# Optimization experiments

Hardware: AMD Instinct MI355X
Metric: run time of the kernel (lower is better)

Reference implementation:

```python
import jax, jax.numpy as jnp
import numpy as np

P = 20000          # plan nodes (queries)
H = 128            # hidden_dim_plan
DIMS = {"table": (100000, 96), "pred": (400000, 160), "agg": (60000, 64), "join": (80000, 64)}
BN_EPS = 1e-5


def setup_inputs() -> dict:
    key = jax.random.key(0)
    ks = iter(jax.random.split(key, 32))
    inp = {}
    for t, (n, d) in DIMS.items():
        inp[f"feat_{t}"] = jax.random.normal(next(ks), (n, d), dtype=jnp.float32)
        inp[f"idx_{t}"] = jax.random.randint(next(ks), (n,), 0, P)
        # per-type encoder: Linear(d, H) (stored as [d, H])
        inp[f"W_{t}"] = jax.random.normal(next(ks), (d, H), dtype=jnp.float32) * 0.02
        inp[f"b_{t}"] = jnp.zeros((H,), jnp.float32)
    # est head: BatchNorm1d(4H) -> Linear(4H,H)+ReLU -> Linear(H,H)+ReLU -> Linear(H,1)
    inp["bn_gamma"] = jnp.ones((4 * H,), jnp.float32)
    inp["bn_beta"] = jnp.zeros((4 * H,), jnp.float32)
    inp["W1"] = jax.random.normal(next(ks), (4 * H, H), dtype=jnp.float32) * 0.02
    inp["b1"] = jnp.zeros((H,), jnp.float32)
    inp["W2"] = jax.random.normal(next(ks), (H, H), dtype=jnp.float32) * 0.02
    inp["b2"] = jnp.zeros((H,), jnp.float32)
    inp["W3"] = jax.random.normal(next(ks), (H, 1), dtype=jnp.float32) * 0.02
    inp["b3"] = jnp.zeros((1,), jnp.float32)
    inp["num_plan"] = P
    return inp


def _seg_mean(x, idx, num_seg):
    # DGL mean pooling: mean over incoming edges, 0 for nodes with no edges
    s = jax.ops.segment_sum(x, idx, num_segments=num_seg)
    c = jax.ops.segment_sum(jnp.ones((x.shape[0], 1), x.dtype), idx, num_segments=num_seg)
    return s / jnp.maximum(c, 1.0)


def _forward(feats, idxs, params, num_plan):
    pooled = []
    for t in ("table", "pred", "agg", "join"):
        enc = jax.nn.relu(feats[t] @ params[f"W_{t}"] + params[f"b_{t}"])  # [N_t, H]
        pooled.append(_seg_mean(enc, idxs[t], num_plan))                    # [P, H]
    x = jnp.concatenate(pooled, axis=1)  # [P, 4H]
    # BatchNorm1d (training mode: batch statistics, biased variance)
    mu = jnp.mean(x, axis=0)
    var = jnp.mean(jnp.square(x - mu), axis=0)
    x = (x - mu) * jax.lax.rsqrt(var + BN_EPS) * params["bn_gamma"] + params["bn_beta"]
    x = jax.nn.relu(x @ params["W1"] + params["b1"])
    x = jax.nn.relu(x @ params["W2"] + params["b2"])
    return x @ params["W3"] + params["b3"]  # [P, 1]


def reference(feat_table, feat_pred, feat_agg, feat_join,
              W_table, b_table, W_pred, b_pred, W_agg, b_agg, W_join, b_join,
              bn_gamma, bn_beta, W1, b1, W2, b2, W3, b3,
              idx_table, idx_pred, idx_agg, idx_join, num_plan):
    feats = {"table": feat_table, "pred": feat_pred, "agg": feat_agg, "join": feat_join}
    idxs = {"table": idx_table, "pred": idx_pred, "agg": idx_agg, "join": idx_join}
    params = dict(W_table=W_table, b_table=b_table, W_pred=W_pred, b_pred=b_pred,
                  W_agg=W_agg, b_agg=b_agg, W_join=W_join, b_join=b_join,
                  bn_gamma=bn_gamma, bn_beta=bn_beta, W1=W1, b1=b1, W2=W2, b2=b2, W3=W3, b3=b3)
    return _forward(feats, idxs, params, num_plan)
```

## Files before the change

kernel.cpp:

```cpp
#include <hip/hip_runtime.h>
#include <cstdint>


constexpr int P_N = 20000;
constexpr int HD  = 128;

typedef __attribute__((ext_vector_type(8))) short  short8v;
typedef __attribute__((ext_vector_type(4))) float  float4v;
typedef __attribute__((ext_vector_type(8))) float  float8v;
typedef __attribute__((ext_vector_type(8))) __bf16 bf16x8;

__device__ inline ushort f2bf(float f) {
    uint32_t u = __builtin_bit_cast(uint32_t, f);
    u += 0x7fffu + ((u >> 16) & 1u);
    return (ushort)(u >> 16);
}
__device__ inline short8v cvt8v(float4 a, float4 b) {
    float8v f = {a.x, a.y, a.z, a.w, b.x, b.y, b.z, b.w};
    bf16x8 h = __builtin_convertvector(f, bf16x8);
    return __builtin_bit_cast(short8v, h);
}
__device__ inline float4v mfma16(short8v a, short8v b, float4v c) {
    return __builtin_amdgcn_mfma_f32_16x16x32_bf16(a, b, c, 0, 0, 0);
}

__global__ void k_count_all(const int* __restrict__ i0, const int* __restrict__ i1,
                            const int* __restrict__ i2, const int* __restrict__ i3,
                            int n0, int n1, int n2, int n3, int* __restrict__ counts) {
    int i = blockIdx.x * blockDim.x + threadIdx.x;
    const int n01 = n0 + n1, n012 = n0 + n1 + n2, tot = n012 + n3;
    if (i >= tot) return;
    int tp, li; const int* p;
    if (i < n0)        { tp = 0; li = i;        p = i0; }
    else if (i < n01)  { tp = 1; li = i - n0;   p = i1; }
    else if (i < n012) { tp = 2; li = i - n01;  p = i2; }
    else               { tp = 3; li = i - n012; p = i3; }
    atomicAdd(&counts[tp * P_N + p[li]], 1);
}

__global__ void k_scan(int* __restrict__ counts_all, int* __restrict__ cur_all,
                       float* __restrict__ invc,
                       int* l0, int* l1, int* l2, int* l3,
                       int* s0, int* s1, int* s2, int* s3,
                       int n0, int n1, int n2, int n3) {
    const int type = blockIdx.x;
    int* counts = counts_all + type * P_N;
    int* curs   = cur_all   + type * P_N;
    float* ic   = invc      + type * P_N;
    const int T = 256;
    const int CH = (P_N + T - 1) / T;
    int t = threadIdx.x;
    __shared__ int sums[T];
    __shared__ int pref[T];
    int local = 0;
    int p0 = t * CH;
    for (int i = 0; i < CH; ++i) {
        int p = p0 + i;
        if (p < P_N) local += counts[p];
    }
    sums[t] = local;
    __syncthreads();
    if (t == 0) {
        int run = 0;
        for (int j = 0; j < T; ++j) { pref[j] = run; run += sums[j]; }
    }
    __syncthreads();
    int run = pref[t];
    for (int i = 0; i < CH; ++i) {
        int p = p0 + i;
        if (p < P_N) {
            int c = counts[p];
            curs[p] = run; run += c;
            ic[p] = 1.f / (float)max(c, 1);
        }
    }
    int N; int *lp, *sp;
    if (type == 0)      { N = n0; lp = l0; sp = s0; }
    else if (type == 1) { N = n1; lp = l1; sp = s1; }
    else if (type == 2) { N = n2; lp = l2; sp = s2; }
    else                { N = n3; lp = l3; sp = s3; }
    if (t < 160) { lp[N + t] = 0; sp[N + t] = -1; }
}

__global__ void k_fill_prepw(const int* __restrict__ i0, const int* __restrict__ i1,
                             const int* __restrict__ i2, const int* __restrict__ i3,
                             int n0, int n1, int n2, int n3, int* __restrict__ cur_all,
                             int* l0, int* l1, int* l2, int* l3,
                             int* s0p, int* s1p, int* s2p, int* s3p,
                             int nb_fill,
                             const float* w0s, const float* w1s, const float* w2s,
                             const float* w3s, const float* w4s, const float* w5s,
                             ushort* d0, ushort* d1, ushort* d2, ushort* d3,
                             ushort* d4, ushort* d5) {
    if (blockIdx.x < (unsigned)nb_fill) {
        int i = blockIdx.x * blockDim.x + threadIdx.x;
        const int n01 = n0 + n1, n012 = n0 + n1 + n2, tot = n012 + n3;
        if (i >= tot) return;
        int tp, li; const int* p; int *lst, *spl;
        if (i < n0)        { tp = 0; li = i;        p = i0; lst = l0; spl = s0p; }
        else if (i < n01)  { tp = 1; li = i - n0;   p = i1; lst = l1; spl = s1p; }
        else if (i < n012) { tp = 2; li = i - n01;  p = i2; lst = l2; spl = s2p; }
        else               { tp = 3; li = i - n012; p = i3; lst = l3; spl = s3p; }
        int pl = p[li];
        int pos = atomicAdd(&cur_all[tp * P_N + pl], 1);
        lst[pos] = li;
        spl[pos] = pl;
    } else {
        int i = (blockIdx.x - nb_fill) * blockDim.x + threadIdx.x;
        const float* s; ushort* d; int Dv, li;
        if (i < 12288)       { s = w0s; d = d0; Dv = 96;  li = i; }
        else if (i < 32768)  { s = w1s; d = d1; Dv = 160; li = i - 12288; }
        else if (i < 40960)  { s = w2s; d = d2; Dv = 64;  li = i - 32768; }
        else if (i < 49152)  { s = w3s; d = d3; Dv = 64;  li = i - 40960; }
        else if (i < 114688) { s = w4s; d = d4; Dv = 512; li = i - 49152; }
        else if (i < 131072) { s = w5s; d = d5; Dv = 128; li = i - 114688; }
        else return;
        int n = li / Dv, k = li - n * Dv;
        d[li] = f2bf(s[k * HD + n]);
    }
}

__device__ __forceinline__ void reduce_group(float (*Cs)[132], const int* plans,
                                             float* __restrict__ x, int toff, int pbase) {
    const int t = threadIdx.x;
    const int col = t & 127, half = t >> 7;
    int curp = -2; float s = 0.f;
    #pragma unroll 8
    for (int r = 0; r < 32; ++r) {
        int p = plans[pbase + half * 32 + r];
        float v = Cs[half * 32 + r][col];
        if (p != curp) {
            if (curp >= 0) atomicAdd(&x[(size_t)curp * 512 + toff + col], s);
            s = 0.f; curp = p;
        }
        if (p >= 0) s += v;
    }
    if (curp >= 0) atomicAdd(&x[(size_t)curp * 512 + toff + col], s);
}

template<int D>
__device__ __forceinline__ void enc_body(
    const float* __restrict__ feat, const ushort* __restrict__ WT,
    const float* __restrict__ bias, const int* __restrict__ list,
    const int* __restrict__ splan, float* __restrict__ x, int toff, int tile,
    float (*Cs)[132], int* plans)
{
    constexpr int NKS = D / 32;
    const int t = threadIdx.x;
    const int w = t >> 6, lane = t & 63;
    const int lq = lane >> 4, lr = lane & 15;
    const int m0 = tile * 128;

    if (t < 128) plans[t] = splan[m0 + t];
    const int l0v = list[m0 + w * 16 + lr];
    const int l1v = list[m0 + 64 + w * 16 + lr];

    const float* a0p = feat + (size_t)l0v * D + lq * 8;
    const float* a1p = feat + (size_t)l1v * D + lq * 8;

    float4 s0[2 * NKS], s1[2 * NKS];
    #pragma unroll
    for (int ks = 0; ks < NKS; ++ks) {
        s0[2 * ks]     = *(const float4*)(a0p + ks * 32);
        s0[2 * ks + 1] = *(const float4*)(a0p + ks * 32 + 4);
    }
    #pragma unroll
    for (int ks = 0; ks < NKS; ++ks) {
        s1[2 * ks]     = *(const float4*)(a1p + ks * 32);
        s1[2 * ks + 1] = *(const float4*)(a1p + ks * 32 + 4);
    }
    short8v a0[NKS], a1[NKS];
    #pragma unroll
    for (int ks = 0; ks < NKS; ++ks) a0[ks] = cvt8v(s0[2 * ks], s0[2 * ks + 1]);
    #pragma unroll
    for (int ks = 0; ks < NKS; ++ks) a1[ks] = cvt8v(s1[2 * ks], s1[2 * ks + 1]);

    float bv[8];
    #pragma unroll
    for (int nf = 0; nf < 8; ++nf) bv[nf] = bias[nf * 16 + lr];

    float4v acc0[8], acc1[8];
    #pragma unroll
    for (int nf = 0; nf < 8; ++nf) {
        acc0[nf] = (float4v){0.f, 0.f, 0.f, 0.f};
        acc1[nf] = (float4v){0.f, 0.f, 0.f, 0.f};
    }

    const ushort* wp = WT + lr * D + lq * 8;
    short8v bcur[8];
    #pragma unroll
    for (int nf = 0; nf < 8; ++nf) bcur[nf] = *(const short8v*)(wp + nf * 16 * D);
    #pragma unroll
    for (int ks = 0; ks < NKS; ++ks) {
        short8v bnxt[8];
        if (ks + 1 < NKS) {
            #pragma unroll
            for (int nf = 0; nf < 8; ++nf)
                bnxt[nf] = *(const short8v*)(wp + nf * 16 * D + (ks + 1) * 32);
        }
        #pragma unroll
        for (int nf = 0; nf < 8; ++nf) acc0[nf] = mfma16(a0[ks], bcur[nf], acc0[nf]);
        #pragma unroll
        for (int nf = 0; nf < 8; ++nf) acc1[nf] = mfma16(a1[ks], bcur[nf], acc1[nf]);
        if (ks + 1 < NKS) {
            #pragma unroll
            for (int nf = 0; nf < 8; ++nf) bcur[nf] = bnxt[nf];
        }
    }

    #pragma unroll
    for (int nf = 0; nf < 8; ++nf) {
        #pragma unroll
        for (int j = 0; j < 4; ++j)
            Cs[w * 16 + lq * 4 + j][nf * 16 + lr] = fmaxf(acc0[nf][j] + bv[nf], 0.f);
    }
    __syncthreads();
    reduce_group(Cs, plans, x, toff, 0);
    __syncthreads();
    #pragma unroll
    for (int nf = 0; nf < 8; ++nf) {
        #pragma unroll
        for (int j = 0; j < 4; ++j)
            Cs[w * 16 + lq * 4 + j][nf * 16 + lr] = fmaxf(acc1[nf][j] + bv[nf], 0.f);
    }
    __syncthreads();
    reduce_group(Cs, plans, x, toff, 64);
}

__global__ __launch_bounds__(256, 2) void k_enc_all(
    const float* f0, const float* f1, const float* f2, const float* f3,
    const ushort* w0, const ushort* w1, const ushort* w2, const ushort* w3,
    const float* b0, const float* b1, const float* b2, const float* b3,
    const int* l0, const int* l1, const int* l2, const int* l3,
    const int* s0, const int* s1, const int* s2, const int* s3,
    float* x, int ntp, int ntt, int nta)
{
    __shared__ float Cs[64][132];
    __shared__ int plans[128];
    int bid = blockIdx.x;
    if (bid < ntp) { enc_body<160>(f1, w1, b1, l1, s1, x, 128, bid, Cs, plans); return; }
    bid -= ntp;
    if (bid < ntt) { enc_body<96>(f0, w0, b0, l0, s0, x, 0, bid, Cs, plans); return; }
    bid -= ntt;
    if (bid < nta) { enc_body<64>(f2, w2, b2, l2, s2, x, 256, bid, Cs, plans); return; }
    bid -= nta;
    enc_body<64>(f3, w3, b3, l3, s3, x, 384, bid, Cs, plans);
}

__global__ __launch_bounds__(512) void k_bnstats(
    const float* __restrict__ x, const float* __restrict__ invc,
    float* __restrict__ bnsum, int* __restrict__ done,
    const float* __restrict__ gamma, const float* __restrict__ beta,
    float* __restrict__ scale, float* __restrict__ shiftv)
{
    const int t = threadIdx.x;
    const int r0 = blockIdx.x * 40;
    const int r1 = min(r0 + 40, P_N);
    const float* ic = invc + (t >> 7) * P_N;
    float s = 0.f, q = 0.f;
    for (int r = r0; r < r1; ++r) {
        float v = x[(size_t)r * 512 + t] * ic[r];
        s += v; q += v * v;
    }
    atomicAdd(&bnsum[t], s);
    atomicAdd(&bnsum[512 + t], q);

    __shared__ int amLast;
    __syncthreads();
    if (t == 0) {
        __threadfence();
        int prev = __hip_atomic_fetch_add(done, 1, __ATOMIC_ACQ_REL, __HIP_MEMORY_SCOPE_AGENT);
        amLast = (prev == (int)gridDim.x - 1);
    }
    __syncthreads();
    if (amLast) {
        const float invn = 1.f / (float)P_N;
        float sm = __hip_atomic_load(&bnsum[t],       __ATOMIC_RELAXED, __HIP_MEMORY_SCOPE_AGENT);
        float sq = __hip_atomic_load(&bnsum[512 + t], __ATOMIC_RELAXED, __HIP_MEMORY_SCOPE_AGENT);
        float mu  = sm * invn;
        float var = sq * invn - mu * mu;
        float rstd = rsqrtf(fmaxf(var, 0.f) + 1e-5f);
        float sc = gamma[t] * rstd;
        scale[t]  = sc;
        shiftv[t] = beta[t] - mu * sc;
    }
}

__global__ __launch_bounds__(256) void k_head(
    const float* __restrict__ x, const float* __restrict__ invc,
    const float* __restrict__ scale, const float* __restrict__ shiftv,
    const ushort* __restrict__ WT1, const float* __restrict__ b1,
    const ushort* __restrict__ WT2, const float* __restrict__ b2,
    const float* __restrict__ W3, const float* __restrict__ b3,
    float* __restrict__ out)
{
    __shared__ float h[2][16][132];
    __shared__ float red[2][32];
    const int t = threadIdx.x;
    const int w = t >> 6, lane = t & 63;
    const int lq = lane >> 4, lr = lane & 15;
    const int wr = w >> 1, wc = w & 1;
    const int p0 = blockIdx.x * 32;
    const int row = p0 + wr * 16 + lr;
    const float* xr = x + (size_t)row * 512;

    float4v acc[4];
    #pragma unroll
    for (int nf = 0; nf < 4; ++nf) acc[nf] = (float4v){0.f, 0.f, 0.f, 0.f};

    #pragma unroll
    for (int kc = 0; kc < 4; ++kc) {
        const float ic = invc[kc * P_N + row];
        float4 st[8];
        #pragma unroll
        for (int k2 = 0; k2 < 4; ++k2) {
            const int k0 = kc * 128 + k2 * 32 + lq * 8;
            st[2 * k2]     = *(const float4*)(xr + k0);
            st[2 * k2 + 1] = *(const float4*)(xr + k0 + 4);
        }
        short8v a[4];
        #pragma unroll
        for (int k2 = 0; k2 < 4; ++k2) {
            const int k0 = kc * 128 + k2 * 32 + lq * 8;
            float4 sc0 = *(const float4*)(scale + k0);
            float4 sc1 = *(const float4*)(scale + k0 + 4);
            float4 sh0 = *(const float4*)(shiftv + k0);
            float4 sh1 = *(const float4*)(shiftv + k0 + 4);
            float4 v0, v1;
            v0.x = st[2*k2].x   * ic * sc0.x + sh0.x;
            v0.y = st[2*k2].y   * ic * sc0.y + sh0.y;
            v0.z = st[2*k2].z   * ic * sc0.z + sh0.z;
            v0.w = st[2*k2].w   * ic * sc0.w + sh0.w;
            v1.x = st[2*k2+1].x * ic * sc1.x + sh1.x;
            v1.y = st[2*k2+1].y * ic * sc1.y + sh1.y;
            v1.z = st[2*k2+1].z * ic * sc1.z + sh1.z;
            v1.w = st[2*k2+1].w * ic * sc1.w + sh1.w;
            a[k2] = cvt8v(v0, v1);
        }
        #pragma unroll
        for (int k2 = 0; k2 < 4; ++k2) {
            const int ks = kc * 4 + k2;
            #pragma unroll
            for (int nf = 0; nf < 4; ++nf) {
                short8v b = *(const short8v*)(WT1 + (size_t)(wc * 64 + nf * 16 + lr) * 512 + ks * 32 + lq * 8);
                acc[nf] = mfma16(a[k2], b, acc[nf]);
            }
        }
    }
    #pragma unroll
    for (int nf = 0; nf < 4; ++nf) {
        const int c = wc * 64 + nf * 16 + lr;
        const float bvv = b1[c];
        #pragma unroll
        for (int j = 0; j < 4; ++j)
            h[wr][lq * 4 + j][c] = fmaxf(acc[nf][j] + bvv, 0.f);
    }
    __syncthreads();

    short8v a2[4];
    #pragma unroll
    for (int ks = 0; ks < 4; ++ks) {
        const float* hp = &h[wr][lr][ks * 32 + lq * 8];
        a2[ks] = cvt8v(*(const float4*)hp, *(const float4*)(hp + 4));
    }
    float4v acc2[4];
    #pragma unroll
    for (int nf = 0; nf < 4; ++nf) acc2[nf] = (float4v){0.f, 0.f, 0.f, 0.f};
    #pragma unroll
    for (int ks = 0; ks < 4; ++ks) {
        #pragma unroll
        for (int nf = 0; nf < 4; ++nf) {
            short8v b = *(const short8v*)(WT2 + (wc * 64 + nf * 16 + lr) * 128 + ks * 32 + lq * 8);
            acc2[nf] = mfma16(a2[ks], b, acc2[nf]);
        }
    }

    float s0 = 0.f, s1 = 0.f, s2 = 0.f, s3 = 0.f;
    #pragma unroll
    for (int nf = 0; nf < 4; ++nf) {
        const int c = wc * 64 + nf * 16 + lr;
        const float w3v = W3[c];
        const float bvv = b2[c];
        s0 += fmaxf(acc2[nf][0] + bvv, 0.f) * w3v;
        s1 += fmaxf(acc2[nf][1] + bvv, 0.f) * w3v;
        s2 += fmaxf(acc2[nf][2] + bvv, 0.f) * w3v;
        s3 += fmaxf(acc2[nf][3] + bvv, 0.f) * w3v;
    }
    #pragma unroll
    for (int o = 1; o < 16; o <<= 1) {
        s0 += __shfl_xor(s0, o);
        s1 += __shfl_xor(s1, o);
        s2 += __shfl_xor(s2, o);
        s3 += __shfl_xor(s3, o);
    }
    if (lr == 0) {
        red[wc][wr * 16 + lq * 4 + 0] = s0;
        red[wc][wr * 16 + lq * 4 + 1] = s1;
        red[wc][wr * 16 + lq * 4 + 2] = s2;
        red[wc][wr * 16 + lq * 4 + 3] = s3;
    }
    __syncthreads();
    if (t < 32) out[p0 + t] = red[0][t] + red[1][t] + b3[0];
}

extern "C" void kernel_launch(void* const* d_in, const int* in_sizes, int n_in,
                              void* d_out, int out_size, void* d_ws, size_t ws_size,
                              hipStream_t stream)
{
    const float* feats[4] = {(const float*)d_in[0], (const float*)d_in[4], (const float*)d_in[8],  (const float*)d_in[12]};
    const int*   idxs[4]  = {(const int*)d_in[1],   (const int*)d_in[5],   (const int*)d_in[9],   (const int*)d_in[13]};
    const float* Ws[4]    = {(const float*)d_in[2], (const float*)d_in[6], (const float*)d_in[10], (const float*)d_in[14]};
    const float* bs[4]    = {(const float*)d_in[3], (const float*)d_in[7], (const float*)d_in[11], (const float*)d_in[15]};
    const float* gamma = (const float*)d_in[16];
    const float* beta  = (const float*)d_in[17];
    const float* W1 = (const float*)d_in[18]; const float* b1 = (const float*)d_in[19];
    const float* W2 = (const float*)d_in[20]; const float* b2 = (const float*)d_in[21];
    const float* W3 = (const float*)d_in[22]; const float* b3 = (const float*)d_in[23];
    int Ns[4] = {in_sizes[1], in_sizes[5], in_sizes[9], in_sizes[13]};

    char* ws = (char*)d_ws;
    int*   counts = (int*)(ws + 0);
    float* bnsum  = (float*)(ws + 320000);
    int*   done   = (int*)(ws + 324096);
    float* x      = (float*)(ws + 324352);
    int*   curs   = (int*)(ws + 41284352);
    int* lists[4];
    lists[0] = (int*)(ws + 41604352);
    lists[1] = (int*)(ws + 42004992);
    lists[2] = (int*)(ws + 43605632);
    lists[3] = (int*)(ws + 43846272);
    int* splans[4];
    splans[0] = (int*)(ws + 44166912);
    splans[1] = (int*)(ws + 44567552);
    splans[2] = (int*)(ws + 46168192);
    splans[3] = (int*)(ws + 46408832);
    ushort* WTs[4];
    WTs[0] = (ushort*)(ws + 46729472);
    WTs[1] = (ushort*)(ws + 46754048);
    WTs[2] = (ushort*)(ws + 46795008);
    WTs[3] = (ushort*)(ws + 46811392);
    float* invc   = (float*)(ws + 46827776);
    ushort* WT1   = (ushort*)(ws + 47147776);
    ushort* WT2   = (ushort*)(ws + 47278848);
    float* scale  = (float*)(ws + 47311616);
    float* shiftv = (float*)(ws + 47313664);

    hipMemsetAsync(ws, 0, 41284352, stream);

    const int tot = Ns[0] + Ns[1] + Ns[2] + Ns[3];
    k_count_all<<<(tot + 255) / 256, 256, 0, stream>>>(
        idxs[0], idxs[1], idxs[2], idxs[3], Ns[0], Ns[1], Ns[2], Ns[3], counts);
    k_scan<<<4, 256, 0, stream>>>(counts, curs, invc,
        lists[0], lists[1], lists[2], lists[3],
        splans[0], splans[1], splans[2], splans[3],
        Ns[0], Ns[1], Ns[2], Ns[3]);
    const int nb_fill = (tot + 255) / 256;
    k_fill_prepw<<<nb_fill + 512, 256, 0, stream>>>(
        idxs[0], idxs[1], idxs[2], idxs[3], Ns[0], Ns[1], Ns[2], Ns[3], curs,
        lists[0], lists[1], lists[2], lists[3],
        splans[0], splans[1], splans[2], splans[3],
        nb_fill,
        Ws[0], Ws[1], Ws[2], Ws[3], W1, W2,
        WTs[0], WTs[1], WTs[2], WTs[3], WT1, WT2);
    const int ntp = (Ns[1] + 127) / 128, ntt = (Ns[0] + 127) / 128;
    const int nta = (Ns[2] + 127) / 128, ntj = (Ns[3] + 127) / 128;
    k_enc_all<<<ntp + ntt + nta + ntj, 256, 0, stream>>>(
        feats[0], feats[1], feats[2], feats[3],
        WTs[0], WTs[1], WTs[2], WTs[3],
        bs[0], bs[1], bs[2], bs[3],
        lists[0], lists[1], lists[2], lists[3],
        splans[0], splans[1], splans[2], splans[3],
        x, ntp, ntt, nta);
    k_bnstats<<<500, 512, 0, stream>>>(x, invc, bnsum, done, gamma, beta, scale, shiftv);
    k_head<<<P_N / 32, 256, 0, stream>>>(x, invc, scale, shiftv,
                                         WT1, b1, WT2, b2, W3, b3, (float*)d_out);
}
```

Baseline: 381.2 us.

## Scatter bf16-converted features into plan-sorted order during fill, drop index lists

The fill kernel now converts each input feature row to bf16 and writes it to its sorted position in a new workspace buffer. The encoder then reads contiguous bf16 rows instead of gathering fp32 rows through a permutation list, and the list buffers are removed. The aim is cheaper, coalesced, half-width loads in the MFMA encoder. The cost is an extra full write and re-read of a bf16 copy of every feature table. The fill kernel's per-thread row copies are also poorly coalesced across threads.

New measurement: 614.7 us. 1.61x slower.

```diff
diff --git a/kernel.cpp b/kernel.cpp
--- a/kernel.cpp
+++ b/kernel.cpp
@@ -40,7 +40,6 @@
 
 __global__ void k_scan(int* __restrict__ counts_all, int* __restrict__ cur_all,
                        float* __restrict__ invc,
-                       int* l0, int* l1, int* l2, int* l3,
                        int* s0, int* s1, int* s2, int* s3,
                        int n0, int n1, int n2, int n3) {
     const int type = blockIdx.x;
@@ -74,37 +73,47 @@
             ic[p] = 1.f / (float)max(c, 1);
         }
     }
-    int N; int *lp, *sp;
-    if (type == 0)      { N = n0; lp = l0; sp = s0; }
-    else if (type == 1) { N = n1; lp = l1; sp = s1; }
-    else if (type == 2) { N = n2; lp = l2; sp = s2; }
-    else                { N = n3; lp = l3; sp = s3; }
-    if (t < 160) { lp[N + t] = 0; sp[N + t] = -1; }
-}
-
-__global__ void k_fill_prepw(const int* __restrict__ i0, const int* __restrict__ i1,
-                             const int* __restrict__ i2, const int* __restrict__ i3,
-                             int n0, int n1, int n2, int n3, int* __restrict__ cur_all,
-                             int* l0, int* l1, int* l2, int* l3,
-                             int* s0p, int* s1p, int* s2p, int* s3p,
-                             int nb_fill,
-                             const float* w0s, const float* w1s, const float* w2s,
-                             const float* w3s, const float* w4s, const float* w5s,
-                             ushort* d0, ushort* d1, ushort* d2, ushort* d3,
-                             ushort* d4, ushort* d5) {
+    int N; int* sp;
+    if (type == 0)      { N = n0; sp = s0; }
+    else if (type == 1) { N = n1; sp = s1; }
+    else if (type == 2) { N = n2; sp = s2; }
+    else                { N = n3; sp = s3; }
+    if (t < 160) sp[N + t] = -1;
+}
+
+__global__ void k_fill_conv_prepw(
+    const int* __restrict__ i0, const int* __restrict__ i1,
+    const int* __restrict__ i2, const int* __restrict__ i3,
+    const float* __restrict__ f0, const float* __restrict__ f1,
+    const float* __restrict__ f2, const float* __restrict__ f3,
+    ushort* g0, ushort* g1, ushort* g2, ushort* g3,
+    int n0, int n1, int n2, int n3, int* __restrict__ cur_all,
+    int* s0p, int* s1p, int* s2p, int* s3p,
+    int nb_fill,
+    const float* w0s, const float* w1s, const float* w2s,
+    const float* w3s, const float* w4s, const float* w5s,
+    ushort* d0, ushort* d1, ushort* d2, ushort* d3,
+    ushort* d4, ushort* d5)
+{
     if (blockIdx.x < (unsigned)nb_fill) {
         int i = blockIdx.x * blockDim.x + threadIdx.x;
         const int n01 = n0 + n1, n012 = n0 + n1 + n2, tot = n012 + n3;
         if (i >= tot) return;
-        int tp, li; const int* p; int *lst, *spl;
-        if (i < n0)        { tp = 0; li = i;        p = i0; lst = l0; spl = s0p; }
-        else if (i < n01)  { tp = 1; li = i - n0;   p = i1; lst = l1; spl = s1p; }
-        else if (i < n012) { tp = 2; li = i - n01;  p = i2; lst = l2; spl = s2p; }
-        else               { tp = 3; li = i - n012; p = i3; lst = l3; spl = s3p; }
+        int tp, li; const int* p; int* spl; const float* fsrc; ushort* gdst; int Dv;
+        if (i < n0)        { tp = 0; li = i;        p = i0; spl = s0p; fsrc = f0; gdst = g0; Dv = 96;  }
+        else if (i < n01)  { tp = 1; li = i - n0;   p = i1; spl = s1p; fsrc = f1; gdst = g1; Dv = 160; }
+        else if (i < n012) { tp = 2; li = i - n01;  p = i2; spl = s2p; fsrc = f2; gdst = g2; Dv = 64;  }
+        else               { tp = 3; li = i - n012; p = i3; spl = s3p; fsrc = f3; gdst = g3; Dv = 64;  }
         int pl = p[li];
         int pos = atomicAdd(&cur_all[tp * P_N + pl], 1);
-        lst[pos] = li;
         spl[pos] = pl;
+        const float* src = fsrc + (size_t)li * Dv;
+        ushort* dst = gdst + (size_t)pos * Dv;
+        for (int u = 0; u < Dv / 8; ++u) {
+            float4 x0 = *(const float4*)(src + u * 8);
+            float4 x1 = *(const float4*)(src + u * 8 + 4);
+            *(short8v*)(dst + u * 8) = cvt8v(x0, x1);
+        }
     } else {
         int i = (blockIdx.x - nb_fill) * blockDim.x + threadIdx.x;
         const float* s; ushort* d; int Dv, li;
@@ -140,9 +149,9 @@
 
 template<int D>
 __device__ __forceinline__ void enc_body(
-    const float* __restrict__ feat, const ushort* __restrict__ WT,
-    const float* __restrict__ bias, const int* __restrict__ list,
-    const int* __restrict__ splan, float* __restrict__ x, int toff, int tile,
+    const ushort* __restrict__ gfeat, const ushort* __restrict__ WT,
+    const float* __restrict__ bias, const int* __restrict__ splan,
+    float* __restrict__ x, int toff, int tile,
     float (*Cs)[132], int* plans)
 {
     constexpr int NKS = D / 32;
@@ -152,28 +161,14 @@
     const int m0 = tile * 128;
 
     if (t < 128) plans[t] = splan[m0 + t];
-    const int l0v = list[m0 + w * 16 + lr];
-    const int l1v = list[m0 + 64 + w * 16 + lr];
-
-    const float* a0p = feat + (size_t)l0v * D + lq * 8;
-    const float* a1p = feat + (size_t)l1v * D + lq * 8;
-
-    float4 s0[2 * NKS], s1[2 * NKS];
-    #pragma unroll
-    for (int ks = 0; ks < NKS; ++ks) {
-        s0[2 * ks]     = *(const float4*)(a0p + ks * 32);
-        s0[2 * ks + 1] = *(const float4*)(a0p + ks * 32 + 4);
-    }
-    #pragma unroll
-    for (int ks = 0; ks < NKS; ++ks) {
-        s1[2 * ks]     = *(const float4*)(a1p + ks * 32);
-        s1[2 * ks + 1] = *(const float4*)(a1p + ks * 32 + 4);
-    }
+
+    const ushort* a0p = gfeat + (size_t)(m0 + w * 16 + lr) * D + lq * 8;
+    const ushort* a1p = gfeat + (size_t)(m0 + 64 + w * 16 + lr) * D + lq * 8;
     short8v a0[NKS], a1[NKS];
     #pragma unroll
-    for (int ks = 0; ks < NKS; ++ks) a0[ks] = cvt8v(s0[2 * ks], s0[2 * ks + 1]);
-    #pragma unroll
-    for (int ks = 0; ks < NKS; ++ks) a1[ks] = cvt8v(s1[2 * ks], s1[2 * ks + 1]);
+    for (int ks = 0; ks < NKS; ++ks) a0[ks] = *(const short8v*)(a0p + ks * 32);
+    #pragma unroll
+    for (int ks = 0; ks < NKS; ++ks) a1[ks] = *(const short8v*)(a1p + ks * 32);
 
     float bv[8];
     #pragma unroll
@@ -228,23 +223,22 @@
 }
 
 __global__ __launch_bounds__(256, 2) void k_enc_all(
-    const float* f0, const float* f1, const float* f2, const float* f3,
+    const ushort* g0, const ushort* g1, const ushort* g2, const ushort* g3,
     const ushort* w0, const ushort* w1, const ushort* w2, const ushort* w3,
     const float* b0, const float* b1, const float* b2, const float* b3,
-    const int* l0, const int* l1, const int* l2, const int* l3,
     const int* s0, const int* s1, const int* s2, const int* s3,
     float* x, int ntp, int ntt, int nta)
 {
     __shared__ float Cs[64][132];
     __shared__ int plans[128];
     int bid = blockIdx.x;
-    if (bid < ntp) { enc_body<160>(f1, w1, b1, l1, s1, x, 128, bid, Cs, plans); return; }
+    if (bid < ntp) { enc_body<160>(g1, w1, b1, s1, x, 128, bid, Cs, plans); return; }
     bid -= ntp;
-    if (bid < ntt) { enc_body<96>(f0, w0, b0, l0, s0, x, 0, bid, Cs, plans); return; }
+    if (bid < ntt) { enc_body< 96>(g0, w0, b0, s0, x, 0,   bid, Cs, plans); return; }
     bid -= ntt;
-    if (bid < nta) { enc_body<64>(f2, w2, b2, l2, s2, x, 256, bid, Cs, plans); return; }
+    if (bid < nta) { enc_body< 64>(g2, w2, b2, s2, x, 256, bid, Cs, plans); return; }
     bid -= nta;
-    enc_body<64>(f3, w3, b3, l3, s3, x, 384, bid, Cs, plans);
+    enc_body<64>(g3, w3, b3, s3, x, 384, bid, Cs, plans);
 }
 
 __global__ __launch_bounds__(512) void k_bnstats(
@@ -424,11 +418,6 @@
     int*   done   = (int*)(ws + 324096);
     float* x      = (float*)(ws + 324352);
     int*   curs   = (int*)(ws + 41284352);
-    int* lists[4];
-    lists[0] = (int*)(ws + 41604352);
-    lists[1] = (int*)(ws + 42004992);
-    lists[2] = (int*)(ws + 43605632);
-    lists[3] = (int*)(ws + 43846272);
     int* splans[4];
     splans[0] = (int*)(ws + 44166912);
     splans[1] = (int*)(ws + 44567552);
@@ -444,6 +433,10 @@
     ushort* WT2   = (ushort*)(ws + 47278848);
     float* scale  = (float*)(ws + 47311616);
     float* shiftv = (float*)(ws + 47313664);
+    ushort* g1 = (ushort*)(ws + 47315712);
+    ushort* g0 = (ushort*)(ws + 175366912);
+    ushort* g2 = (ushort*)(ws + 194597632);
+    ushort* g3 = (ushort*)(ws + 202298112);
 
     hipMemsetAsync(ws, 0, 41284352, stream);
 
@@ -451,13 +444,14 @@
     k_count_all<<<(tot + 255) / 256, 256, 0, stream>>>(
         idxs[0], idxs[1], idxs[2], idxs[3], Ns[0], Ns[1], Ns[2], Ns[3], counts);
     k_scan<<<4, 256, 0, stream>>>(counts, curs, invc,
-        lists[0], lists[1], lists[2], lists[3],
         splans[0], splans[1], splans[2], splans[3],
         Ns[0], Ns[1], Ns[2], Ns[3]);
     const int nb_fill = (tot + 255) / 256;
-    k_fill_prepw<<<nb_fill + 512, 256, 0, stream>>>(
-        idxs[0], idxs[1], idxs[2], idxs[3], Ns[0], Ns[1], Ns[2], Ns[3], curs,
-        lists[0], lists[1], lists[2], lists[3],
+    k_fill_conv_prepw<<<nb_fill + 512, 256, 0, stream>>>(
+        idxs[0], idxs[1], idxs[2], idxs[3],
+        feats[0], feats[1], feats[2], feats[3],
+        g0, g1, g2, g3,
+        Ns[0], Ns[1], Ns[2], Ns[3], curs,
         splans[0], splans[1], splans[2], splans[3],
         nb_fill,
         Ws[0], Ws[1], Ws[2], Ws[3], W1, W2,
@@ -465,10 +459,9 @@
     const int ntp = (Ns[1] + 127) / 128, ntt = (Ns[0] + 127) / 128;
     const int nta = (Ns[2] + 127) / 128, ntj = (Ns[3] + 127) / 128;
     k_enc_all<<<ntp + ntt + nta + ntj, 256, 0, stream>>>(
-        feats[0], feats[1], feats[2], feats[3],
+        g0, g1, g2, g3,
         WTs[0], WTs[1], WTs[2], WTs[3],
         bs[0], bs[1], bs[2], bs[3],
-        lists[0], lists[1], lists[2], lists[3],
         splans[0], splans[1], splans[2], splans[3],
         x, ntp, ntt, nta);
     k_bnstats<<<500, 512, 0, stream>>>(x, invc, bnsum, done, gamma, beta, scale, shiftv);
```

## Split encoder into dense coalesced GEMM and separate sorted gather-pool kernel

Applied to the files above, without the earlier changes.

The encoder GEMM now reads feature rows contiguously instead of gathering them in plan-sorted order, and writes the ReLU'd encodings to a bf16 intermediate buffer. A new pooling kernel then gathers the bf16 rows by the sorted list and does the segmented atomic accumulation into x. The aim is to replace scattered fp32 feature reads with coalesced ones, at the cost of an extra launch plus a write and re-read of about 640k×128 bf16 values. Encodings are also rounded to bf16 before the mean, which adds precision loss.

Result: slower. 471.7 us (+23.8%).

```diff
diff --git a/kernel.cpp b/kernel.cpp
--- a/kernel.cpp
+++ b/kernel.cpp
@@ -22,6 +22,9 @@
 }
 __device__ inline float4v mfma16(short8v a, short8v b, float4v c) {
     return __builtin_amdgcn_mfma_f32_16x16x32_bf16(a, b, c, 0, 0, 0);
+}
+__device__ inline float bf2f(ushort u) {
+    return __builtin_bit_cast(float, (uint32_t)u << 16);
 }
 
 __global__ void k_count_all(const int* __restrict__ i0, const int* __restrict__ i1,
@@ -120,71 +123,37 @@
     }
 }
 
-__device__ __forceinline__ void reduce_group(float (*Cs)[132], const int* plans,
-                                             float* __restrict__ x, int toff, int pbase) {
-    const int t = threadIdx.x;
-    const int col = t & 127, half = t >> 7;
-    int curp = -2; float s = 0.f;
-    #pragma unroll 8
-    for (int r = 0; r < 32; ++r) {
-        int p = plans[pbase + half * 32 + r];
-        float v = Cs[half * 32 + r][col];
-        if (p != curp) {
-            if (curp >= 0) atomicAdd(&x[(size_t)curp * 512 + toff + col], s);
-            s = 0.f; curp = p;
-        }
-        if (p >= 0) s += v;
-    }
-    if (curp >= 0) atomicAdd(&x[(size_t)curp * 512 + toff + col], s);
-}
-
 template<int D>
 __device__ __forceinline__ void enc_body(
     const float* __restrict__ feat, const ushort* __restrict__ WT,
-    const float* __restrict__ bias, const int* __restrict__ list,
-    const int* __restrict__ splan, float* __restrict__ x, int toff, int tile,
-    float (*Cs)[132], int* plans)
+    const float* __restrict__ bias, ushort* __restrict__ eout,
+    int tile, int N, float (*Cs)[132])
 {
     constexpr int NKS = D / 32;
     const int t = threadIdx.x;
     const int w = t >> 6, lane = t & 63;
     const int lq = lane >> 4, lr = lane & 15;
-    const int m0 = tile * 128;
-
-    if (t < 128) plans[t] = splan[m0 + t];
-    const int l0v = list[m0 + w * 16 + lr];
-    const int l1v = list[m0 + 64 + w * 16 + lr];
-
-    const float* a0p = feat + (size_t)l0v * D + lq * 8;
-    const float* a1p = feat + (size_t)l1v * D + lq * 8;
-
-    float4 s0[2 * NKS], s1[2 * NKS];
+    const int m0 = tile * 64;
+
+    const int row = min(m0 + w * 16 + lr, N - 1);
+    const float* ap = feat + (size_t)row * D + lq * 8;
+    float4 st[2 * NKS];
     #pragma unroll
     for (int ks = 0; ks < NKS; ++ks) {
-        s0[2 * ks]     = *(const float4*)(a0p + ks * 32);
-        s0[2 * ks + 1] = *(const float4*)(a0p + ks * 32 + 4);
-    }
-    #pragma unroll
-    for (int ks = 0; ks < NKS; ++ks) {
-        s1[2 * ks]     = *(const float4*)(a1p + ks * 32);
-        s1[2 * ks + 1] = *(const float4*)(a1p + ks * 32 + 4);
-    }
-    short8v a0[NKS], a1[NKS];
-    #pragma unroll
-    for (int ks = 0; ks < NKS; ++ks) a0[ks] = cvt8v(s0[2 * ks], s0[2 * ks + 1]);
-    #pragma unroll
-    for (int ks = 0; ks < NKS; ++ks) a1[ks] = cvt8v(s1[2 * ks], s1[2 * ks + 1]);
+        st[2 * ks]     = *(const float4*)(ap + ks * 32);
+        st[2 * ks + 1] = *(const float4*)(ap + ks * 32 + 4);
+    }
+    short8v a[NKS];
+    #pragma unroll
+    for (int ks = 0; ks < NKS; ++ks) a[ks] = cvt8v(st[2 * ks], st[2 * ks + 1]);
 
     float bv[8];
     #pragma unroll
     for (int nf = 0; nf < 8; ++nf) bv[nf] = bias[nf * 16 + lr];
 
-    float4v acc0[8], acc1[8];
-    #pragma unroll
-    for (int nf = 0; nf < 8; ++nf) {
-        acc0[nf] = (float4v){0.f, 0.f, 0.f, 0.f};
-        acc1[nf] = (float4v){0.f, 0.f, 0.f, 0.f};
-    }
+    float4v acc[8];
+    #pragma unroll
+    for (int nf = 0; nf < 8; ++nf) acc[nf] = (float4v){0.f, 0.f, 0.f, 0.f};
 
     const ushort* wp = WT + lr * D + lq * 8;
     short8v bcur[8];
@@ -199,9 +168,7 @@
                 bnxt[nf] = *(const short8v*)(wp + nf * 16 * D + (ks + 1) * 32);
         }
         #pragma unroll
-        for (int nf = 0; nf < 8; ++nf) acc0[nf] = mfma16(a0[ks], bcur[nf], acc0[nf]);
-        #pragma unroll
-        for (int nf = 0; nf < 8; ++nf) acc1[nf] = mfma16(a1[ks], bcur[nf], acc1[nf]);
+        for (int nf = 0; nf < 8; ++nf) acc[nf] = mfma16(a[ks], bcur[nf], acc[nf]);
         if (ks + 1 < NKS) {
             #pragma unroll
             for (int nf = 0; nf < 8; ++nf) bcur[nf] = bnxt[nf];
@@ -212,39 +179,93 @@
     for (int nf = 0; nf < 8; ++nf) {
         #pragma unroll
         for (int j = 0; j < 4; ++j)
-            Cs[w * 16 + lq * 4 + j][nf * 16 + lr] = fmaxf(acc0[nf][j] + bv[nf], 0.f);
-    }
-    __syncthreads();
-    reduce_group(Cs, plans, x, toff, 0);
-    __syncthreads();
-    #pragma unroll
-    for (int nf = 0; nf < 8; ++nf) {
-        #pragma unroll
-        for (int j = 0; j < 4; ++j)
-            Cs[w * 16 + lq * 4 + j][nf * 16 + lr] = fmaxf(acc1[nf][j] + bv[nf], 0.f);
-    }
-    __syncthreads();
-    reduce_group(Cs, plans, x, toff, 64);
-}
-
-__global__ __launch_bounds__(256, 2) void k_enc_all(
+            Cs[w * 16 + lq * 4 + j][nf * 16 + lr] = fmaxf(acc[nf][j] + bv[nf], 0.f);
+    }
+    __syncthreads();
+
+    const int r = t >> 2, c0 = (t & 3) * 32;
+    if (m0 + r < N) {
+        ushort* dst = eout + (size_t)(m0 + r) * HD + c0;
+        #pragma unroll
+        for (int q = 0; q < 4; ++q) {
+            short8v v;
+            #pragma unroll
+            for (int e = 0; e < 8; ++e) v[e] = (short)f2bf(Cs[r][c0 + q * 8 + e]);
+            *(short8v*)(dst + q * 8) = v;
+        }
+    }
+}
+
+__global__ __launch_bounds__(256, 2) void k_enc_dense(
     const float* f0, const float* f1, const float* f2, const float* f3,
     const ushort* w0, const ushort* w1, const ushort* w2, const ushort* w3,
     const float* b0, const float* b1, const float* b2, const float* b3,
+    ushort* e0, ushort* e1, ushort* e2, ushort* e3,
+    int n0, int n1, int n2, int n3, int ntp, int ntt, int nta)
+{
+    __shared__ float Cs[64][132];
+    int bid = blockIdx.x;
+    if (bid < ntp) { enc_body<160>(f1, w1, b1, e1, bid, n1, Cs); return; }
+    bid -= ntp;
+    if (bid < ntt) { enc_body< 96>(f0, w0, b0, e0, bid, n0, Cs); return; }
+    bid -= ntt;
+    if (bid < nta) { enc_body< 64>(f2, w2, b2, e2, bid, n2, Cs); return; }
+    bid -= nta;
+    enc_body<64>(f3, w3, b3, e3, bid, n3, Cs);
+}
+
+__device__ __forceinline__ void pool_body(
+    const ushort* __restrict__ eout, const int* __restrict__ list,
+    const int* __restrict__ splan, float* __restrict__ x, int toff, int tile,
+    ushort* T, int* plans, int* rows)
+{
+    const int t = threadIdx.x;
+    const int m0 = tile * 128;
+    if (t < 128) {
+        rows[t]  = list[m0 + t];
+        plans[t] = splan[m0 + t];
+    }
+    __syncthreads();
+    #pragma unroll
+    for (int q = 0; q < 8; ++q) {
+        int c = t + q * 256;
+        int r = c >> 4, off = (c & 15) * 8;
+        *(short8v*)(T + r * HD + off) =
+            *(const short8v*)(eout + (size_t)rows[r] * HD + off);
+    }
+    __syncthreads();
+    const int col = t & 127, half = t >> 7;
+    int curp = -2; float s = 0.f;
+    #pragma unroll 8
+    for (int r = half * 64; r < half * 64 + 64; ++r) {
+        int p = plans[r];
+        float v = bf2f(T[r * HD + col]);
+        if (p != curp) {
+            if (curp >= 0) atomicAdd(&x[(size_t)curp * 512 + toff + col], s);
+            s = 0.f; curp = p;
+        }
+        if (p >= 0) s += v;
+    }
+    if (curp >= 0) atomicAdd(&x[(size_t)curp * 512 + toff + col], s);
+}
+
+__global__ __launch_bounds__(256, 4) void k_pool(
+    const ushort* e0, const ushort* e1, const ushort* e2, const ushort* e3,
     const int* l0, const int* l1, const int* l2, const int* l3,
     const int* s0, const int* s1, const int* s2, const int* s3,
     float* x, int ntp, int ntt, int nta)
 {
-    __shared__ float Cs[64][132];
+    __shared__ ushort T[128 * HD];
     __shared__ int plans[128];
+    __shared__ int rows[128];
     int bid = blockIdx.x;
-    if (bid < ntp) { enc_body<160>(f1, w1, b1, l1, s1, x, 128, bid, Cs, plans); return; }
+    if (bid < ntp) { pool_body(e1, l1, s1, x, 128, bid, T, plans, rows); return; }
     bid -= ntp;
-    if (bid < ntt) { enc_body<96>(f0, w0, b0, l0, s0, x, 0, bid, Cs, plans); return; }
+    if (bid < ntt) { pool_body(e0, l0, s0, x, 0,   bid, T, plans, rows); return; }
     bid -= ntt;
-    if (bid < nta) { enc_body<64>(f2, w2, b2, l2, s2, x, 256, bid, Cs, plans); return; }
+    if (bid < nta) { pool_body(e2, l2, s2, x, 256, bid, T, plans, rows); return; }
     bid -= nta;
-    enc_body<64>(f3, w3, b3, l3, s3, x, 384, bid, Cs, plans);
+    pool_body(e3, l3, s3, x, 384, bid, T, plans, rows);
 }
 
 __global__ __launch_bounds__(512) void k_bnstats(
@@ -444,6 +465,10 @@
     ushort* WT2   = (ushort*)(ws + 47278848);
     float* scale  = (float*)(ws + 47311616);
     float* shiftv = (float*)(ws + 47313664);
+    ushort* e1 = (ushort*)(ws + 47315712);
+    ushort* e0 = (ushort*)(ws + 149715712);
+    ushort* e2 = (ushort*)(ws + 175315712);
+    ushort* e3 = (ushort*)(ws + 190675712);
 
     hipMemsetAsync(ws, 0, 41284352, stream);
 
@@ -462,15 +487,25 @@
         nb_fill,
         Ws[0], Ws[1], Ws[2], Ws[3], W1, W2,
         WTs[0], WTs[1], WTs[2], WTs[3], WT1, WT2);
-    const int ntp = (Ns[1] + 127) / 128, ntt = (Ns[0] + 127) / 128;
-    const int nta = (Ns[2] + 127) / 128, ntj = (Ns[3] + 127) / 128;
-    k_enc_all<<<ntp + ntt + nta + ntj, 256, 0, stream>>>(
-        feats[0], feats[1], feats[2], feats[3],
-        WTs[0], WTs[1], WTs[2], WTs[3],
-        bs[0], bs[1], bs[2], bs[3],
-        lists[0], lists[1], lists[2], lists[3],
-        splans[0], splans[1], splans[2], splans[3],
-        x, ntp, ntt, nta);
+    {
+        const int ntp = (Ns[1] + 63) / 64, ntt = (Ns[0] + 63) / 64;
+        const int nta = (Ns[2] + 63) / 64, ntj = (Ns[3] + 63) / 64;
+        k_enc_dense<<<ntp + ntt + nta + ntj, 256, 0, stream>>>(
+            feats[0], feats[1], feats[2], feats[3],
+            WTs[0], WTs[1], WTs[2], WTs[3],
+            bs[0], bs[1], bs[2], bs[3],
+            e0, e1, e2, e3,
+            Ns[0], Ns[1], Ns[2], Ns[3], ntp, ntt, nta);
+    }
+    {
+        const int ntp = (Ns[1] + 127) / 128, ntt = (Ns[0] + 127) / 128;
+        const int nta = (Ns[2] + 127) / 128, ntj = (Ns[3] + 127) / 128;
+        k_pool<<<ntp + ntt + nta + ntj, 256, 0, stream>>>(
+            e0, e1, e2, e3,
+            lists[0], lists[1], lists[2], lists[3],
+            splans[0], splans[1], splans[2], splans[3],
+            x, ntp, ntt, nta);
+    }
     k_bnstats<<<500, 512, 0, stream>>>(x, invc, bnsum, done, gamma, beta, scale, shiftv);
     k_head<<<P_N / 32, 256, 0, stream>>>(x, invc, scale, shiftv,
                                          WT1, b1, WT2, b2, W3, b3, (float*)d_out);
```

## Fuse x zeroing into count kernel and split head MLP across 4 waves per 16 rows

Applied to the files above, without the earlier changes.

The large memset of the pooled x buffer is replaced by zeroing done in extra blocks of the count kernel, so it runs concurrently with the atomic counting and only the small counters are memset. The head kernel now handles 16 rows per block with each of the 4 waves computing 32 output columns, doubling the block count to improve occupancy and parallelism. The cost is that each block rereads the same x rows across waves and reloads more weight fragments overall.

Measured after the change: 384.0 us. Within noise of the previous version (+0.7%).

```diff
diff --git a/kernel.cpp b/kernel.cpp
--- a/kernel.cpp
+++ b/kernel.cpp
@@ -24,18 +24,27 @@
     return __builtin_amdgcn_mfma_f32_16x16x32_bf16(a, b, c, 0, 0, 0);
 }
 
-__global__ void k_count_all(const int* __restrict__ i0, const int* __restrict__ i1,
-                            const int* __restrict__ i2, const int* __restrict__ i3,
-                            int n0, int n1, int n2, int n3, int* __restrict__ counts) {
-    int i = blockIdx.x * blockDim.x + threadIdx.x;
-    const int n01 = n0 + n1, n012 = n0 + n1 + n2, tot = n012 + n3;
-    if (i >= tot) return;
-    int tp, li; const int* p;
-    if (i < n0)        { tp = 0; li = i;        p = i0; }
-    else if (i < n01)  { tp = 1; li = i - n0;   p = i1; }
-    else if (i < n012) { tp = 2; li = i - n01;  p = i2; }
-    else               { tp = 3; li = i - n012; p = i3; }
-    atomicAdd(&counts[tp * P_N + p[li]], 1);
+__global__ void k_count_zero(const int* __restrict__ i0, const int* __restrict__ i1,
+                             const int* __restrict__ i2, const int* __restrict__ i3,
+                             int n0, int n1, int n2, int n3, int* __restrict__ counts,
+                             int nb_count, float4* __restrict__ xz) {
+    if (blockIdx.x < (unsigned)nb_count) {
+        int i = blockIdx.x * blockDim.x + threadIdx.x;
+        const int n01 = n0 + n1, n012 = n0 + n1 + n2, tot = n012 + n3;
+        if (i >= tot) return;
+        int tp, li; const int* p;
+        if (i < n0)        { tp = 0; li = i;        p = i0; }
+        else if (i < n01)  { tp = 1; li = i - n0;   p = i1; }
+        else if (i < n012) { tp = 2; li = i - n01;  p = i2; }
+        else               { tp = 3; li = i - n012; p = i3; }
+        atomicAdd(&counts[tp * P_N + p[li]], 1);
+    } else {
+        const int NZ = P_N * 128;
+        int i = (blockIdx.x - nb_count) * blockDim.x + threadIdx.x;
+        const int stride = 2048 * 256;
+        const float4 z = {0.f, 0.f, 0.f, 0.f};
+        for (; i < NZ; i += stride) xz[i] = z;
+    }
 }
 
 __global__ void k_scan(int* __restrict__ counts_all, int* __restrict__ cur_all,
@@ -294,19 +303,18 @@
     const float* __restrict__ W3, const float* __restrict__ b3,
     float* __restrict__ out)
 {
-    __shared__ float h[2][16][132];
-    __shared__ float red[2][32];
+    __shared__ float h[16][132];
+    __shared__ float red[4][16];
     const int t = threadIdx.x;
     const int w = t >> 6, lane = t & 63;
     const int lq = lane >> 4, lr = lane & 15;
-    const int wr = w >> 1, wc = w & 1;
-    const int p0 = blockIdx.x * 32;
-    const int row = p0 + wr * 16 + lr;
+    const int p0 = blockIdx.x * 16;
+    const int row = p0 + lr;
     const float* xr = x + (size_t)row * 512;
 
-    float4v acc[4];
-    #pragma unroll
-    for (int nf = 0; nf < 4; ++nf) acc[nf] = (float4v){0.f, 0.f, 0.f, 0.f};
+    float4v acc[2];
+    #pragma unroll
+    for (int nf = 0; nf < 2; ++nf) acc[nf] = (float4v){0.f, 0.f, 0.f, 0.f};
 
     #pragma unroll
     for (int kc = 0; kc < 4; ++kc) {
@@ -341,44 +349,44 @@
         for (int k2 = 0; k2 < 4; ++k2) {
             const int ks = kc * 4 + k2;
             #pragma unroll
-            for (int nf = 0; nf < 4; ++nf) {
-                short8v b = *(const short8v*)(WT1 + (size_t)(wc * 64 + nf * 16 + lr) * 512 + ks * 32 + lq * 8);
+            for (int nf = 0; nf < 2; ++nf) {
+                short8v b = *(const short8v*)(WT1 + (size_t)(w * 32 + nf * 16 + lr) * 512 + ks * 32 + lq * 8);
                 acc[nf] = mfma16(a[k2], b, acc[nf]);
             }
         }
     }
     #pragma unroll
-    for (int nf = 0; nf < 4; ++nf) {
-        const int c = wc * 64 + nf * 16 + lr;
+    for (int nf = 0; nf < 2; ++nf) {
+        const int c = w * 32 + nf * 16 + lr;
         const float bvv = b1[c];
         #pragma unroll
         for (int j = 0; j < 4; ++j)
-            h[wr][lq * 4 + j][c] = fmaxf(acc[nf][j] + bvv, 0.f);
+            h[lq * 4 + j][c] = fmaxf(acc[nf][j] + bvv, 0.f);
     }
     __syncthreads();
 
     short8v a2[4];
     #pragma unroll
     for (int ks = 0; ks < 4; ++ks) {
-        const float* hp = &h[wr][lr][ks * 32 + lq * 8];
+        const float* hp = &h[lr][ks * 32 + lq * 8];
         a2[ks] = cvt8v(*(const float4*)hp, *(const float4*)(hp + 4));
     }
-    float4v acc2[4];
-    #pragma unroll
-    for (int nf = 0; nf < 4; ++nf) acc2[nf] = (float4v){0.f, 0.f, 0.f, 0.f};
+    float4v acc2[2];
+    #pragma unroll
+    for (int nf = 0; nf < 2; ++nf) acc2[nf] = (float4v){0.f, 0.f, 0.f, 0.f};
     #pragma unroll
     for (int ks = 0; ks < 4; ++ks) {
         #pragma unroll
-        for (int nf = 0; nf < 4; ++nf) {
-            short8v b = *(const short8v*)(WT2 + (wc * 64 + nf * 16 + lr) * 128 + ks * 32 + lq * 8);
+        for (int nf = 0; nf < 2; ++nf) {
+            short8v b = *(const short8v*)(WT2 + (w * 32 + nf * 16 + lr) * 128 + ks * 32 + lq * 8);
             acc2[nf] = mfma16(a2[ks], b, acc2[nf]);
         }
     }
 
     float s0 = 0.f, s1 = 0.f, s2 = 0.f, s3 = 0.f;
     #pragma unroll
-    for (int nf = 0; nf < 4; ++nf) {
-        const int c = wc * 64 + nf * 16 + lr;
+    for (int nf = 0; nf < 2; ++nf) {
+        const int c = w * 32 + nf * 16 + lr;
         const float w3v = W3[c];
         const float bvv = b2[c];
         s0 += fmaxf(acc2[nf][0] + bvv, 0.f) * w3v;
@@ -394,13 +402,13 @@
         s3 += __shfl_xor(s3, o);
     }
     if (lr == 0) {
-        red[wc][wr * 16 + lq * 4 + 0] = s0;
-        red[wc][wr * 16 + lq * 4 + 1] = s1;
-        red[wc][wr * 16 + lq * 4 + 2] = s2;
-        red[wc][wr * 16 + lq * 4 + 3] = s3;
-    }
-    __syncthreads();
-    if (t < 32) out[p0 + t] = red[0][t] + red[1][t] + b3[0];
+        red[w][lq * 4 + 0] = s0;
+        red[w][lq * 4 + 1] = s1;
+        red[w][lq * 4 + 2] = s2;
+        red[w][lq * 4 + 3] = s3;
+    }
+    __syncthreads();
+    if (t < 16) out[p0 + t] = red[0][t] + red[1][t] + red[2][t] + red[3][t] + b3[0];
 }
 
 extern "C" void kernel_launch(void* const* d_in, const int* in_sizes, int n_in,
@@ -445,11 +453,13 @@
     float* scale  = (float*)(ws + 47311616);
     float* shiftv = (float*)(ws + 47313664);
 
-    hipMemsetAsync(ws, 0, 41284352, stream);
+    hipMemsetAsync(ws, 0, 324352, stream);
 
     const int tot = Ns[0] + Ns[1] + Ns[2] + Ns[3];
-    k_count_all<<<(tot + 255) / 256, 256, 0, stream>>>(
-        idxs[0], idxs[1], idxs[2], idxs[3], Ns[0], Ns[1], Ns[2], Ns[3], counts);
+    const int nb_count = (tot + 255) / 256;
+    k_count_zero<<<nb_count + 2048, 256, 0, stream>>>(
+        idxs[0], idxs[1], idxs[2], idxs[3], Ns[0], Ns[1], Ns[2], Ns[3], counts,
+        nb_count, (float4*)x);
     k_scan<<<4, 256, 0, stream>>>(counts, curs, invc,
         lists[0], lists[1], lists[2], lists[3],
         splans[0], splans[1], splans[2], splans[3],
@@ -472,6 +482,6 @@
         splans[0], splans[1], splans[2], splans[3],
         x, ntp, ntt, nta);
     k_bnstats<<<500, 512, 0, stream>>>(x, invc, bnsum, done, gamma, beta, scale, shiftv);
-    k_head<<<P_N / 32, 256, 0, stream>>>(x, invc, scale, shiftv,
+    k_head<<<P_N / 16, 256, 0, stream>>>(x, invc, scale, shiftv,
                                          WT1, b1, WT2, b2, W3, b3, (float*)d_out);
 }
```
